# Performance work log

Hardware: AMD Instinct MI355X
Metric: run time of the kernel (lower is better)

The kernel has to match this reference:

```python
import jax, jax.numpy as jnp
import numpy as np


def setup_inputs() -> dict:
    key = jax.random.key(0)
    k1, k2, k3 = jax.random.split(key, 3)
    B, C, D, S = 16, 80, 1024, 14  # batch, num_classes, feature dim, conv size
    return {
        "batch_size": B,
        "img_feature_map": jax.random.normal(k1, (B, D, S, S), dtype=jnp.float32),
        "word_features": jax.random.normal(k2, (C, D), dtype=jnp.float32),
        "fc_a_w": jax.random.normal(k3, (D,), dtype=jnp.float32) / np.float32(np.sqrt(D)),
        "fc_a_b": jnp.zeros((), dtype=jnp.float32),
    }


def reference(batch_size, img_feature_map, word_features, fc_a_w, fc_a_b):
    # img_feature_map: [B, D, H, W] -> [B, H, W, D]
    img = jnp.transpose(img_feature_map, (0, 2, 3, 1))
    # class-wise gated feature: tanh(img * word) -> [B, H, W, C, D]
    gated = jnp.tanh(img[:, :, :, None, :] * word_features[None, None, None, :, :])
    # rank-1 linear score: [B, H, W, C]
    scores = jnp.einsum('bhwcd,d->bhwc', gated, fc_a_w) + fc_a_b
    B, H, W, C = scores.shape
    # softmax over spatial positions (H*W) per (batch, class)
    coef = jax.nn.softmax(scores.reshape(B, H * W, C), axis=1).reshape(B, H, W, C)
    # attention-weighted spatial pooling -> [B, C, D]
    return jnp.einsum('bhwc,bhwd->bcd', coef, img)
```

## Files before the change

### kernel.cpp

```cpp
#include <hip/hip_runtime.h>

#define BB 16
#define CC 80
#define DD 1024
#define HW 196
#define NSP (BB * HW)
#define NCH 8
#define DCH 128
#define CPB 4
#define NCQ (CC / CPB)
#define PG 16
#define PT 8
#define TWO_LOG2E 2.8853900817779268f

__global__ __launch_bounds__(256) void scores_k(const float* __restrict__ img,
                                                const float* __restrict__ word,
                                                const float* __restrict__ fa,
                                                float* __restrict__ partial,
                                                float* __restrict__ imgT) {
    const int g = blockIdx.x * 256 + threadIdx.x;
    if (g >= NSP) return;
    const int b  = g / HW;
    const int hw = g - b * HW;
    const int d0 = blockIdx.y * DCH;
    const int c0 = blockIdx.z * CPB;

    const float* ip = img + ((size_t)b * DD + d0) * HW + hw;

    float p[CPB];
#pragma unroll
    for (int k = 0; k < CPB; ++k) p[k] = 0.f;

    for (int q = 0; q < DCH / 32; ++q) {
        float iv[32];
        const float* qp = ip + (size_t)q * 32 * HW;
#pragma unroll
        for (int i = 0; i < 32; ++i)
            iv[i] = qp[(size_t)i * HW];

        if (blockIdx.z == 0) {
            float4* tp = (float4*)(imgT + (size_t)g * DD + d0 + q * 32);
#pragma unroll
            for (int i = 0; i < 8; ++i)
                tp[i] = make_float4(iv[4 * i], iv[4 * i + 1], iv[4 * i + 2], iv[4 * i + 3]);
        }

#pragma unroll
        for (int i = 0; i < 32; ++i)
            iv[i] *= TWO_LOG2E;

        const float* fp = fa + d0 + q * 32;
#pragma unroll
        for (int k = 0; k < CPB; ++k) {
            const float* wp = word + (size_t)(c0 + k) * DD + d0 + q * 32;
            float p0 = 0.f, p1 = 0.f;
#pragma unroll
            for (int i = 0; i < 32; i += 2) {
                float y0 = iv[i]     * wp[i];
                float y1 = iv[i + 1] * wp[i + 1];
                float e0 = __builtin_amdgcn_exp2f(y0);
                float e1 = __builtin_amdgcn_exp2f(y1);
                float r0 = __builtin_amdgcn_rcpf(e0 + 1.f);
                float r1 = __builtin_amdgcn_rcpf(e1 + 1.f);
                p0 = fmaf(fp[i],     r0, p0);
                p1 = fmaf(fp[i + 1], r1, p1);
            }
            p[k] += p0 + p1;
        }
    }

#pragma unroll
    for (int k = 0; k < CPB; ++k)
        partial[(((size_t)b * NCH + blockIdx.y) * CC + (c0 + k)) * HW + hw]
            = (-TWO_LOG2E) * p[k];
}

__global__ __launch_bounds__(256) void pool3_k(const float* __restrict__ imgT,
                                               const float* __restrict__ partial,
                                               float* __restrict__ out) {
    __shared__ float ct[PG * HW];
    const int b  = blockIdx.x;
    const int d0 = blockIdx.y * 128;
    const int cg = blockIdx.z * PG;
    const int t  = threadIdx.x;
    const int w  = t >> 6, l = t & 63;

#pragma unroll
    for (int rr = 0; rr < 4; ++rr) {
        const int r = 4 * w + rr;
        const int c = cg + r;
        float x0 = 0.f, x1 = 0.f, x2 = 0.f, x3 = 0.f;
#pragma unroll
        for (int ch = 0; ch < NCH; ++ch) {
            const float* pp = partial + (((size_t)b * NCH + ch) * CC + c) * HW;
            x0 += pp[l];
            x1 += pp[l + 64];
            x2 += pp[l + 128];
            if (l < HW - 192) x3 += pp[l + 192];
        }
        float x3m = (l < HW - 192) ? x3 : -3.4e38f;

        float m = fmaxf(fmaxf(x0, x1), fmaxf(x2, x3m));
#pragma unroll
        for (int off = 32; off >= 1; off >>= 1) m = fmaxf(m, __shfl_xor(m, off, 64));

        float e0 = __builtin_amdgcn_exp2f(x0 - m);
        float e1 = __builtin_amdgcn_exp2f(x1 - m);
        float e2 = __builtin_amdgcn_exp2f(x2 - m);
        float e3 = (l < HW - 192) ? __builtin_amdgcn_exp2f(x3 - m) : 0.f;

        float s = (e0 + e1) + (e2 + e3);
#pragma unroll
        for (int off = 32; off >= 1; off >>= 1) s += __shfl_xor(s, off, 64);

        float inv = __builtin_amdgcn_rcpf(s);
        float* cr = ct + r * HW;
        cr[l]       = e0 * inv;
        cr[l + 64]  = e1 * inv;
        cr[l + 128] = e2 * inv;
        if (l < HW - 192) cr[l + 192] = e3 * inv;
    }
    __syncthreads();

    const float* ib = imgT + (size_t)b * HW * DD + d0 + 2 * l;
    const float* cr0 = ct + (4 * w) * HW;

    float2 a0 = {0, 0}, a1 = {0, 0}, a2 = {0, 0}, a3 = {0, 0};
    for (int h = 0; h < HW; h += 4) {
        float2 i0 = *(const float2*)(ib + (size_t)(h    ) * DD);
        float2 i1 = *(const float2*)(ib + (size_t)(h + 1) * DD);
        float2 i2 = *(const float2*)(ib + (size_t)(h + 2) * DD);
        float2 i3 = *(const float2*)(ib + (size_t)(h + 3) * DD);
        float4 c0v = *(const float4*)(cr0 + h);
        float4 c1v = *(const float4*)(cr0 + HW + h);
        float4 c2v = *(const float4*)(cr0 + 2 * HW + h);
        float4 c3v = *(const float4*)(cr0 + 3 * HW + h);
#define ACC2(A, CV)                                                              \
        A.x = fmaf(CV.x, i0.x, fmaf(CV.y, i1.x, fmaf(CV.z, i2.x, fmaf(CV.w, i3.x, A.x)))); \
        A.y = fmaf(CV.x, i0.y, fmaf(CV.y, i1.y, fmaf(CV.z, i2.y, fmaf(CV.w, i3.y, A.y))));
        ACC2(a0, c0v)
        ACC2(a1, c1v)
        ACC2(a2, c2v)
        ACC2(a3, c3v)
#undef ACC2
    }

    float* ob = out + ((size_t)b * CC + cg + 4 * w) * DD + d0 + 2 * l;
    *(float2*)(ob)                  = a0;
    *(float2*)(ob + DD)             = a1;
    *(float2*)(ob + 2 * (size_t)DD) = a2;
    *(float2*)(ob + 3 * (size_t)DD) = a3;
}

extern "C" void kernel_launch(void* const* d_in, const int* in_sizes, int n_in,
                              void* d_out, int out_size, void* d_ws, size_t ws_size,
                              hipStream_t stream) {
    const float* img  = (const float*)d_in[1];
    const float* word = (const float*)d_in[2];
    const float* fa   = (const float*)d_in[3];
    float* out = (float*)d_out;

    float* partial = (float*)d_ws;
    float* imgT    = partial + (size_t)BB * NCH * CC * HW;

    scores_k<<<dim3((NSP + 255) / 256, NCH, NCQ), 256, 0, stream>>>(img, word, fa, partial, imgT);
    pool3_k<<<dim3(BB, PT, CC / PG), 256, 0, stream>>>(imgT, partial, out);
}
```

Before: 161.9 us.

## Split softmax into separate kernel and double classes per scores block

Moves the partial-sum reduction and softmax out of the pooling kernel into a dedicated softmax kernel that runs once per (batch, class). Before, each of the 8 d-tile blocks of the pooling kernel recomputed it. The pooling kernel now only copies precomputed coefficients into shared memory. Separately, the scores kernel processes 8 classes per block instead of 4, which halves the redundant image reloads but raises register pressure. The cost is an extra kernel launch and a global round trip for the coefficients.

```diff
diff --git a/kernel.cpp b/kernel.cpp
--- a/kernel.cpp
+++ b/kernel.cpp
@@ -7,10 +7,9 @@
 #define NSP (BB * HW)
 #define NCH 8
 #define DCH 128
-#define CPB 4
+#define CPB 8
 #define NCQ (CC / CPB)
 #define PG 16
-#define PT 8
 #define TWO_LOG2E 2.8853900817779268f
 
 __global__ __launch_bounds__(256) void scores_k(const float* __restrict__ img,
@@ -75,7 +74,43 @@
             = (-TWO_LOG2E) * p[k];
 }
 
-__global__ __launch_bounds__(256) void pool3_k(const float* __restrict__ imgT,
+__global__ __launch_bounds__(256) void softmax_k(float* __restrict__ partial) {
+    const int bc = blockIdx.x;
+    const int b = bc / CC, c = bc - b * CC;
+    const int t = threadIdx.x;
+
+    float x = -3.4e38f;
+    if (t < HW) {
+        float P = 0.f;
+#pragma unroll
+        for (int ch = 0; ch < NCH; ++ch)
+            P += partial[(((size_t)b * NCH + ch) * CC + c) * HW + t];
+        x = P;
+    }
+
+    __shared__ float rmax[4], rsum[4];
+    const int wv = t >> 6;
+
+    float m = x;
+#pragma unroll
+    for (int off = 32; off >= 1; off >>= 1) m = fmaxf(m, __shfl_xor(m, off, 64));
+    if ((t & 63) == 0) rmax[wv] = m;
+    __syncthreads();
+    m = fmaxf(fmaxf(rmax[0], rmax[1]), fmaxf(rmax[2], rmax[3]));
+
+    float e = (t < HW) ? __builtin_amdgcn_exp2f(x - m) : 0.f;
+    float s = e;
+#pragma unroll
+    for (int off = 32; off >= 1; off >>= 1) s += __shfl_xor(s, off, 64);
+    if ((t & 63) == 0) rsum[wv] = s;
+    __syncthreads();
+    s = rsum[0] + rsum[1] + rsum[2] + rsum[3];
+
+    if (t < HW)
+        partial[((size_t)b * NCH * CC + c) * HW + t] = e * __builtin_amdgcn_rcpf(s);
+}
+
+__global__ __launch_bounds__(256) void pool4_k(const float* __restrict__ imgT,
                                                const float* __restrict__ partial,
                                                float* __restrict__ out) {
     __shared__ float ct[PG * HW];
@@ -85,44 +120,12 @@
     const int t  = threadIdx.x;
     const int w  = t >> 6, l = t & 63;
 
-#pragma unroll
-    for (int rr = 0; rr < 4; ++rr) {
-        const int r = 4 * w + rr;
-        const int c = cg + r;
-        float x0 = 0.f, x1 = 0.f, x2 = 0.f, x3 = 0.f;
-#pragma unroll
-        for (int ch = 0; ch < NCH; ++ch) {
-            const float* pp = partial + (((size_t)b * NCH + ch) * CC + c) * HW;
-            x0 += pp[l];
-            x1 += pp[l + 64];
-            x2 += pp[l + 128];
-            if (l < HW - 192) x3 += pp[l + 192];
-        }
-        float x3m = (l < HW - 192) ? x3 : -3.4e38f;
-
-        float m = fmaxf(fmaxf(x0, x1), fmaxf(x2, x3m));
-#pragma unroll
-        for (int off = 32; off >= 1; off >>= 1) m = fmaxf(m, __shfl_xor(m, off, 64));
-
-        float e0 = __builtin_amdgcn_exp2f(x0 - m);
-        float e1 = __builtin_amdgcn_exp2f(x1 - m);
-        float e2 = __builtin_amdgcn_exp2f(x2 - m);
-        float e3 = (l < HW - 192) ? __builtin_amdgcn_exp2f(x3 - m) : 0.f;
-
-        float s = (e0 + e1) + (e2 + e3);
-#pragma unroll
-        for (int off = 32; off >= 1; off >>= 1) s += __shfl_xor(s, off, 64);
-
-        float inv = __builtin_amdgcn_rcpf(s);
-        float* cr = ct + r * HW;
-        cr[l]       = e0 * inv;
-        cr[l + 64]  = e1 * inv;
-        cr[l + 128] = e2 * inv;
-        if (l < HW - 192) cr[l + 192] = e3 * inv;
-    }
+    const float4* cs = (const float4*)(partial + ((size_t)b * NCH * CC + cg) * HW);
+    float4* cd = (float4*)ct;
+    for (int j = t; j < PG * HW / 4; j += 256) cd[j] = cs[j];
     __syncthreads();
 
-    const float* ib = imgT + (size_t)b * HW * DD + d0 + 2 * l;
+    const float* ib  = imgT + (size_t)b * HW * DD + d0 + 2 * l;
     const float* cr0 = ct + (4 * w) * HW;
 
     float2 a0 = {0, 0}, a1 = {0, 0}, a2 = {0, 0}, a3 = {0, 0};
@@ -164,5 +167,6 @@
     float* imgT    = partial + (size_t)BB * NCH * CC * HW;
 
     scores_k<<<dim3((NSP + 255) / 256, NCH, NCQ), 256, 0, stream>>>(img, word, fa, partial, imgT);
-    pool3_k<<<dim3(BB, PT, CC / PG), 256, 0, stream>>>(imgT, partial, out);
+    softmax_k<<<BB * CC, 256, 0, stream>>>(partial);
+    pool4_k<<<dim3(BB, NCH, CC / PG), 256, 0, stream>>>(imgT, partial, out);
 }
```

After: 169.7 us. 4.8% more time.
